# Kernel tuning notes

Measured on AMD Instinct MI355X. Metric: run time of the kernel, lower is better.

Reference implementation:

```python
import jax, jax.numpy as jnp
import numpy as np
from jax import lax

S = 1024   # max_num_segments
CB = 25    # color_hist_bins
TB = 10    # texture_hist_bins
EPS = 1e-12


def setup_inputs() -> dict:
    key = jax.random.key(0)
    k1, k2, k3, k4 = jax.random.split(key, 4)
    B, C, R, H, W = 8, 3, 8, 512, 512
    img = jax.random.normal(k1, (B, C, H, W), jnp.float32)
    imgs_bins = jax.random.randint(k2, (B, C, H, W), 0, CB, jnp.int32)
    grads_bins = jax.random.randint(k3, (B, C, R, H, W), 0, TB, jnp.int32)
    reg_lab = jax.random.randint(k4, (B, H, W), 0, S, jnp.int32)
    return {"img": img, "imgs_bins": imgs_bins, "grads_bins": grads_bins, "reg_lab": reg_lab}


def reference(img, imgs_bins, grads_bins, reg_lab):
    B, C, H, W = img.shape
    R = grads_bins.shape[2]
    HW = H * W
    lab = reg_lab.astype(jnp.int32)

    # ---- area_per_segment: scatter_add of ones over flattened labels ----
    flat = (lab.reshape(B, HW) + (jnp.arange(B, dtype=jnp.int32) * S)[:, None]).reshape(-1)
    area = jnp.zeros(B * S, jnp.int32).at[flat].add(1).reshape(B, S)

    # ---- bbox_per_segment: scatter amin/amax of pixel coordinates ----
    yy, xx = jnp.meshgrid(jnp.arange(H, dtype=jnp.int32),
                          jnp.arange(W, dtype=jnp.int32), indexing='ij')
    xb = jnp.broadcast_to(xx.reshape(HW), (B, HW)).reshape(-1)
    yb = jnp.broadcast_to(yy.reshape(HW), (B, HW)).reshape(-1)
    xmin = jnp.full(B * S, W, jnp.int32).at[flat].min(xb)
    ymin = jnp.full(B * S, H, jnp.int32).at[flat].min(yb)
    xmax = jnp.zeros(B * S, jnp.int32).at[flat].max(xb)
    ymax = jnp.zeros(B * S, jnp.int32).at[flat].max(yb)
    # torch does xywh[2:] -= xywh[:2] (no +1), so w = xmax - xmin
    bbox_xywh = jnp.stack([xmin, ymin, xmax - xmin, ymax - ymin], -1).reshape(B, S, 4)

    area_f = area.astype(jnp.float32)

    # ---- color histogram: scatter_add of ones into [B,C,S*CB] ----
    ci = (lab[:, None, :, :] * CB + imgs_bins).reshape(B * C, HW)
    ci = (ci + (jnp.arange(B * C, dtype=jnp.int32) * (S * CB))[:, None]).reshape(-1)
    color_hist = jnp.zeros(B * C * S * CB, jnp.float32).at[ci].add(1.0).reshape(B, C, S, CB)
    color_hist = color_hist.transpose(0, 2, 1, 3).reshape(B, S, C * CB)  # [B,S,C*CB]
    color_hist = color_hist / (area_f * float(C) + EPS)[..., None]

    # ---- texture histogram: scatter_add of ones into [B,C,R,S*TB] ----
    ti = (lab[:, None, None, :, :] * TB + grads_bins).reshape(B * C * R, HW)
    ti = (ti + (jnp.arange(B * C * R, dtype=jnp.int32) * (S * TB))[:, None]).reshape(-1)
    texture_hist = jnp.zeros(B * C * R * S * TB, jnp.float32).at[ti].add(1.0).reshape(B, C, R, S, TB)
    texture_hist = texture_hist.transpose(0, 3, 1, 2, 4).reshape(B, S, C * R * TB)  # [B,S,C*R*TB]
    texture_hist = texture_hist / (area_f * float(C * R) + EPS)[..., None]

    # ---- image_scharr_gradients: depthwise-style conv2d, padding=1 ----
    sx = jnp.array([[-3., 0., 3.], [-10., 0., 10.], [-3., 0., 3.]], jnp.float32)
    kern = jnp.stack([sx, sx.T])[:, None]  # [2,1,3,3]
    grads = lax.conv_general_dilated(img.reshape(B * C, 1, H, W), kern, (1, 1), 'SAME',
                                     dimension_numbers=('NCHW', 'OIHW', 'NCHW'))
    grads = grads.reshape(B, C, 2, H, W)

    return area, bbox_xywh, color_hist, texture_hist, grads
```

## Files before the change

kernel.cpp:

```cpp
#include <hip/hip_runtime.h>

#define B_ 8
#define C_ 3
#define R_ 8
#define H_ 512
#define W_ 512
#define HW_ (H_*W_)
#define S_ 1024
#define CB_ 25
#define TB_ 10

#define O_AREA 0
#define O_BBOX 8192
#define O_COLOR 40960
#define O_TEX 655360
#define O_GRADS 2621440
#define OUT_TOT 15204352

#define NBBOX 8
#define NTEX (B_*C_*R_)
#define NCOL (B_*C_)
#define NHIST (NBBOX + NTEX + NCOL)
#define NCONV 1024
#define NGRID (NHIST + NCONV)

#define PK_WORDS 1048576
#define NEED_WS ((size_t)PK_WORDS * 4)
#define SCR_OFF (OUT_TOT - PK_WORDS)
#define CONV_SAFE (22 << 18)
#define CONV_ALL  (24 << 18)

__global__ __launch_bounds__(1024) void k_pack(const int* __restrict__ lab,
                                               unsigned* __restrict__ plab) {
  const int i = blockIdx.x * 1024 + threadIdx.x;
  const int4 a = ((const int4*)lab)[2 * i];
  const int4 b = ((const int4*)lab)[2 * i + 1];
  uint4 o;
  o.x = (unsigned)(a.x) | ((unsigned)a.y << 16);
  o.y = (unsigned)(a.z) | ((unsigned)a.w << 16);
  o.z = (unsigned)(b.x) | ((unsigned)b.y << 16);
  o.w = (unsigned)(b.z) | ((unsigned)b.w << 16);
  ((uint4*)plab)[i] = o;
}

__global__ __launch_bounds__(1024) void k_fused(
    const float* __restrict__ img,
    const int* __restrict__ imgs_bins,
    const int* __restrict__ grads_bins,
    const unsigned* __restrict__ plab,
    float* __restrict__ out,
    int convHi) {
  __shared__ unsigned smem[12800];
  const int bid = blockIdx.x;
  const int tid = threadIdx.x;

  if (bid < NBBOX) {
    const int b = bid;
    int* mn = (int*)smem;
    mn[tid] = W_; mn[S_ + tid] = H_; mn[2*S_ + tid] = 0; mn[3*S_ + tid] = 0;
    __syncthreads();
    const uint4* lp = (const uint4*)(plab + (size_t)b * (HW_/2));
    for (int t = tid; t < HW_/8; t += 1024) {
      const uint4 L = lp[t];
      const int p = t * 8;
      const int y = p >> 9;
      const int x = p & (W_ - 1);
      #define BBX(l, xx) { const int ll = (int)(l); \
        atomicMin(&mn[ll], xx);        atomicMin(&mn[S_ + ll], y); \
        atomicMax(&mn[2*S_ + ll], xx); atomicMax(&mn[3*S_ + ll], y); }
      BBX(L.x & 0xFFFFu, x)     BBX(L.x >> 16, x + 1)
      BBX(L.y & 0xFFFFu, x + 2) BBX(L.y >> 16, x + 3)
      BBX(L.z & 0xFFFFu, x + 4) BBX(L.z >> 16, x + 5)
      BBX(L.w & 0xFFFFu, x + 6) BBX(L.w >> 16, x + 7)
      #undef BBX
    }
    __syncthreads();
    {
      const int xmn = mn[tid], ymn = mn[S_ + tid];
      const int xmx = mn[2*S_ + tid], ymx = mn[3*S_ + tid];
      float4 v;
      v.x = (float)xmn; v.y = (float)ymn;
      v.z = (float)(xmx - xmn); v.w = (float)(ymx - ymn);
      ((float4*)(out + O_BBOX))[b * S_ + tid] = v;
    }
  } else if (bid < NBBOX + NTEX) {
    const int plane = bid - NBBOX;
    const int b = plane / (C_*R_);
    const int cr = plane - b * (C_*R_);
    int* h = (int*)smem;
    for (int i = tid; i < S_*TB_; i += 1024) h[i] = 0;
    __syncthreads();
    const int4* bp = (const int4*)(grads_bins + (size_t)plane * HW_);
    const uint4* lp = (const uint4*)(plab + (size_t)b * (HW_/2));
    for (int t = tid; t < HW_/8; t += 1024) {
      const uint4 L = lp[t];
      const int4 b0 = bp[2*t];
      const int4 b1 = bp[2*t + 1];
      atomicAdd(&h[(int)(L.x & 0xFFFFu)*TB_ + b0.x], 1);
      atomicAdd(&h[(int)(L.x >> 16)*TB_ + b0.y], 1);
      atomicAdd(&h[(int)(L.y & 0xFFFFu)*TB_ + b0.z], 1);
      atomicAdd(&h[(int)(L.y >> 16)*TB_ + b0.w], 1);
      atomicAdd(&h[(int)(L.z & 0xFFFFu)*TB_ + b1.x], 1);
      atomicAdd(&h[(int)(L.z >> 16)*TB_ + b1.y], 1);
      atomicAdd(&h[(int)(L.w & 0xFFFFu)*TB_ + b1.z], 1);
      atomicAdd(&h[(int)(L.w >> 16)*TB_ + b1.w], 1);
    }
    __syncthreads();
    {
      const int base = tid * TB_;
      int s = 0;
      #pragma unroll
      for (int t = 0; t < TB_; ++t) s += h[base + t];
      const float inv = 1.0f / ((float)s * 24.0f + 1e-12f);
      float* o = out + O_TEX + (size_t)b * (S_ * 240) + tid * 240 + cr * TB_;
      #pragma unroll
      for (int t = 0; t < TB_; ++t) o[t] = (float)h[base + t] * inv;
      if (cr == 0) out[O_AREA + b * S_ + tid] = (float)s;
    }
  } else if (bid < NHIST) {
    const int plane = bid - NBBOX - NTEX;
    const int b = plane / C_;
    const int c = plane - b * C_;
    unsigned* h = smem;
    for (int i = tid; i < (S_*CB_)/2; i += 1024) h[i] = 0;
    __syncthreads();
    const int4* bp = (const int4*)(imgs_bins + (size_t)plane * HW_);
    const uint4* lp = (const uint4*)(plab + (size_t)b * (HW_/2));
    for (int t = tid; t < HW_/8; t += 1024) {
      const uint4 L = lp[t];
      const int4 b0 = bp[2*t];
      const int4 b1 = bp[2*t + 1];
      #define CADD(l, bin) { const int j = (int)(l)*CB_ + (bin); \
        atomicAdd(&h[j >> 1], 1u << ((j & 1) << 4)); }
      CADD(L.x & 0xFFFFu, b0.x) CADD(L.x >> 16, b0.y)
      CADD(L.y & 0xFFFFu, b0.z) CADD(L.y >> 16, b0.w)
      CADD(L.z & 0xFFFFu, b1.x) CADD(L.z >> 16, b1.y)
      CADD(L.w & 0xFFFFu, b1.z) CADD(L.w >> 16, b1.w)
      #undef CADD
    }
    __syncthreads();
    {
      int s = 0;
      #pragma unroll
      for (int ci = 0; ci < CB_; ++ci) {
        const int j = tid * CB_ + ci;
        s += (int)((h[j >> 1] >> ((j & 1) << 4)) & 0xFFFFu);
      }
      const float inv = 1.0f / ((float)s * 3.0f + 1e-12f);
      float* o = out + O_COLOR + (size_t)b * (S_ * 75) + tid * 75 + c * CB_;
      #pragma unroll
      for (int ci = 0; ci < CB_; ++ci) {
        const int j = tid * CB_ + ci;
        o[ci] = (float)((h[j >> 1] >> ((j & 1) << 4)) & 0xFFFFu) * inv;
      }
    }
  } else {
    const int cb = bid - NHIST;
    for (int i = cb * 1024 + tid; i < convHi; i += NCONV * 1024) {
      const int pix = i & (HW_ - 1);
      const int bc = i >> 18;
      const int x = pix & (W_ - 1);
      const int y = pix >> 9;
      const float* im = img + (size_t)bc * HW_;
      const bool xm = x > 0, xp = x < W_ - 1, ym = y > 0, yp = y < H_ - 1;
      const float i00 = (ym && xm) ? im[pix - W_ - 1] : 0.f;
      const float i01 = ym ? im[pix - W_] : 0.f;
      const float i02 = (ym && xp) ? im[pix - W_ + 1] : 0.f;
      const float i10 = xm ? im[pix - 1] : 0.f;
      const float i12 = xp ? im[pix + 1] : 0.f;
      const float i20 = (yp && xm) ? im[pix + W_ - 1] : 0.f;
      const float i21 = yp ? im[pix + W_] : 0.f;
      const float i22 = (yp && xp) ? im[pix + W_ + 1] : 0.f;
      const float gx = 3.f*(i02 - i00) + 10.f*(i12 - i10) + 3.f*(i22 - i20);
      const float gy = 3.f*(i20 - i00) + 10.f*(i21 - i01) + 3.f*(i22 - i02);
      out[O_GRADS + (size_t)(bc*2 + 0)*HW_ + pix] = gx;
      out[O_GRADS + (size_t)(bc*2 + 1)*HW_ + pix] = gy;
    }
  }
}

__global__ __launch_bounds__(1024) void k_conv_tail(const float* __restrict__ img,
                                                    float* __restrict__ out) {
  const int i = CONV_SAFE + blockIdx.x * 1024 + threadIdx.x;
  const int pix = i & (HW_ - 1);
  const int bc = i >> 18;
  const int x = pix & (W_ - 1);
  const int y = pix >> 9;
  const float* im = img + (size_t)bc * HW_;
  const bool xm = x > 0, xp = x < W_ - 1, ym = y > 0, yp = y < H_ - 1;
  const float i00 = (ym && xm) ? im[pix - W_ - 1] : 0.f;
  const float i01 = ym ? im[pix - W_] : 0.f;
  const float i02 = (ym && xp) ? im[pix - W_ + 1] : 0.f;
  const float i10 = xm ? im[pix - 1] : 0.f;
  const float i12 = xp ? im[pix + 1] : 0.f;
  const float i20 = (yp && xm) ? im[pix + W_ - 1] : 0.f;
  const float i21 = yp ? im[pix + W_] : 0.f;
  const float i22 = (yp && xp) ? im[pix + W_ + 1] : 0.f;
  const float gx = 3.f*(i02 - i00) + 10.f*(i12 - i10) + 3.f*(i22 - i20);
  const float gy = 3.f*(i20 - i00) + 10.f*(i21 - i01) + 3.f*(i22 - i02);
  out[O_GRADS + (size_t)(bc*2 + 0)*HW_ + pix] = gx;
  out[O_GRADS + (size_t)(bc*2 + 1)*HW_ + pix] = gy;
}

extern "C" void kernel_launch(void* const* d_in, const int* in_sizes, int n_in,
                              void* d_out, int out_size, void* d_ws, size_t ws_size,
                              hipStream_t stream) {
  const float* img = (const float*)d_in[0];
  const int* imgs_bins = (const int*)d_in[1];
  const int* grads_bins = (const int*)d_in[2];
  const int* reg_lab = (const int*)d_in[3];
  float* out = (float*)d_out;

  const bool ws_ok = ws_size >= NEED_WS;
  unsigned* plab = ws_ok ? (unsigned*)d_ws : (unsigned*)(out + SCR_OFF);
  const int convHi = ws_ok ? CONV_ALL : CONV_SAFE;

  hipLaunchKernelGGL(k_pack, dim3(256), dim3(1024), 0, stream, reg_lab, plab);
  hipLaunchKernelGGL(k_fused, dim3(NGRID), dim3(1024), 0, stream,
                     img, imgs_bins, grads_bins, plab, out, convHi);
  if (!ws_ok) {
    hipLaunchKernelGGL(k_conv_tail, dim3(512), dim3(1024), 0, stream, img, out);
  }
}
```

Measured before the change: 78.21 us.

## Split fused histogram/conv kernel into separate histogram and conv launches

Separates the Scharr gradient work from the histogram/bbox kernel into its own grid-stride kernel launched after the histogram kernel. This removes per-block branch dispatch and the workspace-dependent tail kernel, and it simplifies scheduling. It gives up the concurrency where conv blocks filled CUs left idle by the 224 long-running histogram blocks, so the two phases now run back to back.

```diff
diff --git a/kernel.cpp b/kernel.cpp
--- a/kernel.cpp
+++ b/kernel.cpp
@@ -21,14 +21,12 @@
 #define NTEX (B_*C_*R_)
 #define NCOL (B_*C_)
 #define NHIST (NBBOX + NTEX + NCOL)
+
 #define NCONV 1024
-#define NGRID (NHIST + NCONV)
 
 #define PK_WORDS 1048576
 #define NEED_WS ((size_t)PK_WORDS * 4)
 #define SCR_OFF (OUT_TOT - PK_WORDS)
-#define CONV_SAFE (22 << 18)
-#define CONV_ALL  (24 << 18)
 
 __global__ __launch_bounds__(1024) void k_pack(const int* __restrict__ lab,
                                                unsigned* __restrict__ plab) {
@@ -43,13 +41,11 @@
   ((uint4*)plab)[i] = o;
 }
 
-__global__ __launch_bounds__(1024) void k_fused(
-    const float* __restrict__ img,
+__global__ __launch_bounds__(1024) void k_hist(
     const int* __restrict__ imgs_bins,
     const int* __restrict__ grads_bins,
     const unsigned* __restrict__ plab,
-    float* __restrict__ out,
-    int convHi) {
+    float* __restrict__ out) {
   __shared__ unsigned smem[12800];
   const int bid = blockIdx.x;
   const int tid = threadIdx.x;
@@ -117,7 +113,7 @@
       for (int t = 0; t < TB_; ++t) o[t] = (float)h[base + t] * inv;
       if (cr == 0) out[O_AREA + b * S_ + tid] = (float)s;
     }
-  } else if (bid < NHIST) {
+  } else {
     const int plane = bid - NBBOX - NTEX;
     const int b = plane / C_;
     const int c = plane - b * C_;
@@ -154,52 +150,32 @@
         o[ci] = (float)((h[j >> 1] >> ((j & 1) << 4)) & 0xFFFFu) * inv;
       }
     }
-  } else {
-    const int cb = bid - NHIST;
-    for (int i = cb * 1024 + tid; i < convHi; i += NCONV * 1024) {
-      const int pix = i & (HW_ - 1);
-      const int bc = i >> 18;
-      const int x = pix & (W_ - 1);
-      const int y = pix >> 9;
-      const float* im = img + (size_t)bc * HW_;
-      const bool xm = x > 0, xp = x < W_ - 1, ym = y > 0, yp = y < H_ - 1;
-      const float i00 = (ym && xm) ? im[pix - W_ - 1] : 0.f;
-      const float i01 = ym ? im[pix - W_] : 0.f;
-      const float i02 = (ym && xp) ? im[pix - W_ + 1] : 0.f;
-      const float i10 = xm ? im[pix - 1] : 0.f;
-      const float i12 = xp ? im[pix + 1] : 0.f;
-      const float i20 = (yp && xm) ? im[pix + W_ - 1] : 0.f;
-      const float i21 = yp ? im[pix + W_] : 0.f;
-      const float i22 = (yp && xp) ? im[pix + W_ + 1] : 0.f;
-      const float gx = 3.f*(i02 - i00) + 10.f*(i12 - i10) + 3.f*(i22 - i20);
-      const float gy = 3.f*(i20 - i00) + 10.f*(i21 - i01) + 3.f*(i22 - i02);
-      out[O_GRADS + (size_t)(bc*2 + 0)*HW_ + pix] = gx;
-      out[O_GRADS + (size_t)(bc*2 + 1)*HW_ + pix] = gy;
-    }
   }
 }
 
-__global__ __launch_bounds__(1024) void k_conv_tail(const float* __restrict__ img,
-                                                    float* __restrict__ out) {
-  const int i = CONV_SAFE + blockIdx.x * 1024 + threadIdx.x;
-  const int pix = i & (HW_ - 1);
-  const int bc = i >> 18;
-  const int x = pix & (W_ - 1);
-  const int y = pix >> 9;
-  const float* im = img + (size_t)bc * HW_;
-  const bool xm = x > 0, xp = x < W_ - 1, ym = y > 0, yp = y < H_ - 1;
-  const float i00 = (ym && xm) ? im[pix - W_ - 1] : 0.f;
-  const float i01 = ym ? im[pix - W_] : 0.f;
-  const float i02 = (ym && xp) ? im[pix - W_ + 1] : 0.f;
-  const float i10 = xm ? im[pix - 1] : 0.f;
-  const float i12 = xp ? im[pix + 1] : 0.f;
-  const float i20 = (yp && xm) ? im[pix + W_ - 1] : 0.f;
-  const float i21 = yp ? im[pix + W_] : 0.f;
-  const float i22 = (yp && xp) ? im[pix + W_ + 1] : 0.f;
-  const float gx = 3.f*(i02 - i00) + 10.f*(i12 - i10) + 3.f*(i22 - i20);
-  const float gy = 3.f*(i20 - i00) + 10.f*(i21 - i01) + 3.f*(i22 - i02);
-  out[O_GRADS + (size_t)(bc*2 + 0)*HW_ + pix] = gx;
-  out[O_GRADS + (size_t)(bc*2 + 1)*HW_ + pix] = gy;
+__global__ __launch_bounds__(1024) void k_conv(const float* __restrict__ img,
+                                               float* __restrict__ out) {
+  const int tot = B_*C_*HW_;
+  for (int i = blockIdx.x * 1024 + threadIdx.x; i < tot; i += NCONV * 1024) {
+    const int pix = i & (HW_ - 1);
+    const int bc = i >> 18;
+    const int x = pix & (W_ - 1);
+    const int y = pix >> 9;
+    const float* im = img + (size_t)bc * HW_;
+    const bool xm = x > 0, xp = x < W_ - 1, ym = y > 0, yp = y < H_ - 1;
+    const float i00 = (ym && xm) ? im[pix - W_ - 1] : 0.f;
+    const float i01 = ym ? im[pix - W_] : 0.f;
+    const float i02 = (ym && xp) ? im[pix - W_ + 1] : 0.f;
+    const float i10 = xm ? im[pix - 1] : 0.f;
+    const float i12 = xp ? im[pix + 1] : 0.f;
+    const float i20 = (yp && xm) ? im[pix + W_ - 1] : 0.f;
+    const float i21 = yp ? im[pix + W_] : 0.f;
+    const float i22 = (yp && xp) ? im[pix + W_ + 1] : 0.f;
+    const float gx = 3.f*(i02 - i00) + 10.f*(i12 - i10) + 3.f*(i22 - i20);
+    const float gy = 3.f*(i20 - i00) + 10.f*(i21 - i01) + 3.f*(i22 - i02);
+    out[O_GRADS + (size_t)(bc*2 + 0)*HW_ + pix] = gx;
+    out[O_GRADS + (size_t)(bc*2 + 1)*HW_ + pix] = gy;
+  }
 }
 
 extern "C" void kernel_launch(void* const* d_in, const int* in_sizes, int n_in,
@@ -213,12 +189,9 @@
 
   const bool ws_ok = ws_size >= NEED_WS;
   unsigned* plab = ws_ok ? (unsigned*)d_ws : (unsigned*)(out + SCR_OFF);
-  const int convHi = ws_ok ? CONV_ALL : CONV_SAFE;
 
   hipLaunchKernelGGL(k_pack, dim3(256), dim3(1024), 0, stream, reg_lab, plab);
-  hipLaunchKernelGGL(k_fused, dim3(NGRID), dim3(1024), 0, stream,
-                     img, imgs_bins, grads_bins, plab, out, convHi);
-  if (!ws_ok) {
-    hipLaunchKernelGGL(k_conv_tail, dim3(512), dim3(1024), 0, stream, img, out);
-  }
+  hipLaunchKernelGGL(k_hist, dim3(NHIST), dim3(1024), 0, stream,
+                     imgs_bins, grads_bins, plab, out);
+  hipLaunchKernelGGL(k_conv, dim3(NCONV), dim3(1024), 0, stream, img, out);
 }
```

After: 90.03 us. 1.15x slower.
